# Performance work log

Measured on AMD Instinct MI355X. Metric: run time of the kernel, lower is better.

The kernel has to match this reference:

```python
import jax, jax.numpy as jnp
import numpy as np
import math

N_HEAD = 16
D_MODEL = 1024
D_HEAD = 64
GRID = 28


def _alibi_slopes(heads):
    def pow2(n):
        start = 2 ** (-(2 ** (-(math.log2(n) - 3))))
        return [start * (start ** i) for i in range(n)]
    if math.log2(heads).is_integer():
        return pow2(heads)
    c = 2 ** math.floor(math.log2(heads))
    return pow2(c) + pow2(2 * c)[0::2][: heads - c]


def _teeth_bias(heads):
    # bias[i,j] = |i%14 - j%14| + |i//14 - j//14| (loop in get_bias overwrites the -|j-i| init)
    idx = np.arange(GRID)
    row, col = idx // 14, idx % 14
    b = np.abs(col[:, None] - col[None, :]) + np.abs(row[:, None] - row[None, :])  # [28,28]
    slopes = np.asarray(_alibi_slopes(heads), dtype=np.float32)  # [h]
    return jnp.asarray(slopes[:, None, None] * b[None].astype(np.float32))  # [h,28,28]


def _layer_norm(x, gamma, beta, eps=1e-5):
    mu = jnp.mean(x, axis=-1, keepdims=True)
    var = jnp.var(x, axis=-1, keepdims=True)
    return (x - mu) * jax.lax.rsqrt(var + eps) * gamma + beta


def setup_inputs() -> dict:
    key = jax.random.key(0)
    ks = jax.random.split(key, 6)
    s = 0.02
    return {
        "hidden": jax.random.normal(ks[0], (2048, GRID, D_MODEL), dtype=jnp.float32),
        "wq": jax.random.normal(ks[1], (D_MODEL, N_HEAD * D_HEAD), dtype=jnp.float32) * s,
        "wk": jax.random.normal(ks[2], (D_MODEL, N_HEAD * D_HEAD), dtype=jnp.float32) * s,
        "wv": jax.random.normal(ks[3], (D_MODEL, N_HEAD * D_HEAD), dtype=jnp.float32) * s,
        "wo": jax.random.normal(ks[4], (N_HEAD * D_HEAD, D_MODEL), dtype=jnp.float32) * s,
        "gamma": jnp.ones((D_MODEL,), dtype=jnp.float32),
        "beta": jnp.zeros((D_MODEL,), dtype=jnp.float32),
    }


def reference(hidden, wq, wk, wv, wo, gamma, beta):
    b, s, _ = hidden.shape
    # pre_lnorm: hidden is reassigned to LN(hidden); combined == hidden (memory=None)
    h = _layer_norm(hidden, gamma, beta)
    q = (h @ wq).reshape(b, s, N_HEAD, D_HEAD).transpose(0, 2, 1, 3)  # [b,h,s,d]
    k = (h @ wk).reshape(b, s, N_HEAD, D_HEAD).transpose(0, 2, 1, 3)
    v = (h @ wv).reshape(b, s, N_HEAD, D_HEAD).transpose(0, 2, 1, 3)
    # NOTE: original forward never applies atten_scale -> unscaled dots (faithful)
    scores = jnp.einsum("bhid,bhjd->bhij", q, k)
    scores = scores + _teeth_bias(N_HEAD)[None, :, :s, :s]
    attn = jax.nn.softmax(scores, axis=-1)
    ctx = jnp.einsum("bhij,bhjd->bhid", attn, v)
    ctx = ctx.transpose(0, 2, 1, 3).reshape(b, s, N_HEAD * D_HEAD)
    out = ctx @ wo
    return h + out  # pre_lnorm residual uses the normalized hidden
```

## Files before the change

### kernel.cpp

```cpp
#include <hip/hip_runtime.h>
#include <hip/hip_bf16.h>

typedef unsigned short u16;
typedef __attribute__((ext_vector_type(8))) short bf16x8;
typedef __attribute__((ext_vector_type(4))) float f32x4;

#define DEVINL __device__ __forceinline__

DEVINL u16 f2b(float f) {
    __hip_bfloat16 h = __float2bfloat16(f);
    return __builtin_bit_cast(u16, h);
}
DEVINL float b2f(u16 u) {
    unsigned int x = ((unsigned int)u) << 16;
    return __builtin_bit_cast(float, x);
}
DEVINL int iabs(int x) { return x < 0 ? -x : x; }

#define GL2LDS(g, s)                                                                     \
    __builtin_amdgcn_global_load_lds(                                                    \
        (const __attribute__((address_space(1))) unsigned int*)(g),                      \
        (__attribute__((address_space(3))) unsigned int*)(s), 16, 0, 0)

__global__ __launch_bounds__(256) void wconv_kernel(const float* __restrict__ wq,
                                                    const float* __restrict__ wk,
                                                    const float* __restrict__ wv,
                                                    const float* __restrict__ wo,
                                                    u16* __restrict__ wqkvt,
                                                    u16* __restrict__ wot) {
    __shared__ float tile[32][33];
    int z = blockIdx.z;
    const float* src = (z == 0) ? wq : (z == 1) ? wk : (z == 2) ? wv : wo;
    int n0 = blockIdx.x * 32, k0 = blockIdx.y * 32;
    int r0 = threadIdx.x >> 5, c = threadIdx.x & 31;
#pragma unroll
    for (int i = 0; i < 4; i++) {
        int r = r0 + i * 8;
        tile[r][c] = src[(size_t)(k0 + r) * 1024 + n0 + c];
    }
    __syncthreads();
    u16* dst = (z < 3) ? (wqkvt + (size_t)z * 1024 * 1024) : wot;
#pragma unroll
    for (int i = 0; i < 4; i++) {
        int r = r0 + i * 8;
        dst[(size_t)(n0 + r) * 1024 + k0 + c] = f2b(tile[c][r]);
    }
}

__global__ __launch_bounds__(256) void ln_kernel(const float* __restrict__ x,
                                                 const float* __restrict__ gamma,
                                                 const float* __restrict__ beta,
                                                 u16* __restrict__ h) {
    int w = threadIdx.x >> 6, l = threadIdx.x & 63;
    size_t row = (size_t)blockIdx.x * 4 + w;
    const float4* xr = (const float4*)(x + row * 1024);
    float4 v[4];
    float s = 0.f, sq = 0.f;
#pragma unroll
    for (int i = 0; i < 4; i++) {
        v[i] = xr[l + i * 64];
        s += v[i].x + v[i].y + v[i].z + v[i].w;
        sq += v[i].x * v[i].x + v[i].y * v[i].y + v[i].z * v[i].z + v[i].w * v[i].w;
    }
#pragma unroll
    for (int off = 1; off < 64; off <<= 1) {
        s += __shfl_xor(s, off);
        sq += __shfl_xor(sq, off);
    }
    float mu = s * (1.f / 1024.f);
    float var = sq * (1.f / 1024.f) - mu * mu;
    float rstd = rsqrtf(var + 1e-5f);
    const float4* g4 = (const float4*)gamma;
    const float4* b4 = (const float4*)beta;
#pragma unroll
    for (int i = 0; i < 4; i++) {
        float4 g = g4[l + i * 64], b = b4[l + i * 64];
        float y0 = (v[i].x - mu) * rstd * g.x + b.x;
        float y1 = (v[i].y - mu) * rstd * g.y + b.y;
        float y2 = (v[i].z - mu) * rstd * g.z + b.z;
        float y3 = (v[i].w - mu) * rstd * g.w + b.w;
        unsigned int lo = (unsigned int)f2b(y0) | ((unsigned int)f2b(y1) << 16);
        unsigned int hi = (unsigned int)f2b(y2) | ((unsigned int)f2b(y3) << 16);
        uint2 pk;
        pk.x = lo;
        pk.y = hi;
        *(uint2*)(h + row * 1024 + (size_t)(l + i * 64) * 4) = pk;
    }
}

template <int OUT_BF16, int RESID>
__global__ __launch_bounds__(256, 2) void gemm_bt(const u16* __restrict__ A,
                                                  const u16* __restrict__ Bt,
                                                  void* __restrict__ Cv,
                                                  const u16* __restrict__ resid,
                                                  int lda, int ldc) {
    __shared__ u16 smem[16384];
    int t = threadIdx.x;

    int nwg = gridDim.x;
    int cpx = nwg >> 3;
    int wg = (blockIdx.x & 7) * cpx + (blockIdx.x >> 3);
    const int sgrp = 448 * 8;
    int sn = wg / sgrp;
    int rem = wg - sn * sgrp;
    int bm = rem >> 3;
    int bn = sn * 8 + (rem & 7);

    const char* Ab = (const char*)A;
    const char* Bb = (const char*)Bt;
    size_t aoffg[4], boffg[4];
#pragma unroll
    for (int i = 0; i < 4; i++) {
        int p = t * 16 + i * 4096;
        int row = p >> 7;
        int colb = (p & 127) ^ ((row & 7) << 4);
        aoffg[i] = (size_t)(bm * 128 + row) * (size_t)lda * 2 + colb;
        boffg[i] = (size_t)(bn * 128 + row) * 2048 + colb;
    }
    char* sA = (char*)smem;
    char* sB = sA + 16384;

    int l = t & 63, w = t >> 6;
    int wm = w >> 1, wn = w & 1, g = l >> 4, lr = l & 15;
    int swz = (lr & 7) << 4;

    f32x4 acc[4][4];
#pragma unroll
    for (int m = 0; m < 4; m++)
#pragma unroll
        for (int n = 0; n < 4; n++) acc[m][n] = {0.f, 0.f, 0.f, 0.f};

    for (int kt = 0; kt < 16; ++kt) {
        int kb = kt * 128;
#pragma unroll
        for (int i = 0; i < 4; i++) GL2LDS(Ab + aoffg[i] + kb, sA + i * 4096 + t * 16);
#pragma unroll
        for (int i = 0; i < 4; i++) GL2LDS(Bb + boffg[i] + kb, sB + i * 4096 + t * 16);
        __syncthreads();
#pragma unroll
        for (int ks = 0; ks < 2; ++ks) {
            bf16x8 af[4], bfv[4];
#pragma unroll
            for (int m = 0; m < 4; m++)
                af[m] = *(const bf16x8*)(sA + (wm * 64 + m * 16 + lr) * 128 +
                                         ((ks * 64 + g * 16) ^ swz));
#pragma unroll
            for (int n = 0; n < 4; n++)
                bfv[n] = *(const bf16x8*)(sB + (wn * 64 + n * 16 + lr) * 128 +
                                          ((ks * 64 + g * 16) ^ swz));
#pragma unroll
            for (int m = 0; m < 4; m++)
#pragma unroll
                for (int n = 0; n < 4; n++)
                    acc[m][n] =
                        __builtin_amdgcn_mfma_f32_16x16x32_bf16(af[m], bfv[n], acc[m][n], 0, 0, 0);
        }
        __syncthreads();
    }

    size_t row0 = (size_t)bm * 128 + wm * 64;
    int col0 = bn * 128 + wn * 64;
    if (OUT_BF16) {
        u16* C = (u16*)Cv;
#pragma unroll
        for (int m = 0; m < 4; m++)
#pragma unroll
            for (int n = 0; n < 4; n++)
#pragma unroll
                for (int r = 0; r < 4; r++) {
                    size_t rr = row0 + m * 16 + g * 4 + r;
                    int cc = col0 + n * 16 + lr;
                    C[rr * (size_t)ldc + cc] = f2b(acc[m][n][r]);
                }
    } else {
        float* C = (float*)Cv;
#pragma unroll
        for (int m = 0; m < 4; m++)
#pragma unroll
            for (int n = 0; n < 4; n++)
#pragma unroll
                for (int r = 0; r < 4; r++) {
                    size_t rr = row0 + m * 16 + g * 4 + r;
                    int cc = col0 + n * 16 + lr;
                    float o = acc[m][n][r];
                    if (RESID) o += b2f(resid[rr * 1024 + cc]);
                    C[rr * (size_t)ldc + cc] = o;
                }
    }
}

__global__ __launch_bounds__(256) void attn_kernel(u16* __restrict__ qkv) {
    __shared__ u16 sq[32][264];
    __shared__ u16 sk[32][264];
    __shared__ u16 svt[256][40];
    __shared__ u16 sp[4][32][40];

    int t = threadIdx.x;
    int b = blockIdx.x >> 2, hg = blockIdx.x & 3;
    u16* base = qkv + (size_t)b * 28 * 3072 + hg * 256;

    {
        int rhalf = t >> 7;
        int c2 = (t & 127) * 2;
        for (int it = 0; it < 14; ++it) {
            int row = it * 2 + rhalf;
            const u16* src = base + (size_t)row * 3072;
            unsigned int qv = *(const unsigned int*)(src + c2);
            *(unsigned int*)&sq[row][c2] = qv;
            unsigned int kv = *(const unsigned int*)(src + 1024 + c2);
            *(unsigned int*)&sk[row][c2] = kv;
            unsigned int vv = *(const unsigned int*)(src + 2048 + c2);
            svt[c2][row] = (u16)(vv & 0xffffu);
            svt[c2 + 1][row] = (u16)(vv >> 16);
        }
#pragma unroll
        for (int r = 28; r < 32; ++r) {
            sq[r][t] = 0;
            sk[r][t] = 0;
        }
#pragma unroll
        for (int j = 28; j < 32; ++j) svt[t][j] = 0;
    }
    __syncthreads();

    int w = t >> 6, l = t & 63, g = l >> 4, lr = l & 15;
    int head = hg * 4 + w;

    f32x4 acc[2][2];
#pragma unroll
    for (int a = 0; a < 2; a++)
#pragma unroll
        for (int c = 0; c < 2; c++) acc[a][c] = {0.f, 0.f, 0.f, 0.f};
#pragma unroll
    for (int c = 0; c < 2; c++) {
        int d0 = w * 64 + c * 32 + g * 8;
        bf16x8 a0 = *(const bf16x8*)&sq[lr][d0];
        bf16x8 a1 = *(const bf16x8*)&sq[16 + lr][d0];
        bf16x8 b0 = *(const bf16x8*)&sk[lr][d0];
        bf16x8 b1 = *(const bf16x8*)&sk[16 + lr][d0];
        acc[0][0] = __builtin_amdgcn_mfma_f32_16x16x32_bf16(a0, b0, acc[0][0], 0, 0, 0);
        acc[0][1] = __builtin_amdgcn_mfma_f32_16x16x32_bf16(a0, b1, acc[0][1], 0, 0, 0);
        acc[1][0] = __builtin_amdgcn_mfma_f32_16x16x32_bf16(a1, b0, acc[1][0], 0, 0, 0);
        acc[1][1] = __builtin_amdgcn_mfma_f32_16x16x32_bf16(a1, b1, acc[1][1], 0, 0, 0);
    }

    float slope = exp2f(-0.5f * (float)(head + 1));
    int j0 = lr, j1 = 16 + lr;
    int j0m = j0 % 14, j0d = j0 / 14;
    int j1m = j1 % 14, j1d = j1 / 14;
#pragma unroll
    for (int it = 0; it < 2; ++it) {
#pragma unroll
        for (int r = 0; r < 4; ++r) {
            int i = it * 16 + g * 4 + r;
            int im = i % 14, id = i / 14;
            float s0 = acc[it][0][r] + slope * (float)(iabs(im - j0m) + iabs(id - j0d));
            float s1 = (j1 < 28)
                           ? acc[it][1][r] + slope * (float)(iabs(im - j1m) + iabs(id - j1d))
                           : -1e30f;
            float mx = fmaxf(s0, s1);
#pragma unroll
            for (int off = 1; off < 16; off <<= 1) mx = fmaxf(mx, __shfl_xor(mx, off));
            float e0 = __expf(s0 - mx), e1 = __expf(s1 - mx);
            float sm = e0 + e1;
#pragma unroll
            for (int off = 1; off < 16; off <<= 1) sm += __shfl_xor(sm, off);
            float inv = 1.f / sm;
            sp[w][i][lr] = f2b(e0 * inv);
            sp[w][i][16 + lr] = f2b(e1 * inv);
        }
    }
    __syncthreads();

    bf16x8 pa0 = *(const bf16x8*)&sp[w][lr][g * 8];
    bf16x8 pa1 = *(const bf16x8*)&sp[w][16 + lr][g * 8];
    f32x4 o[2][4];
#pragma unroll
    for (int a = 0; a < 2; a++)
#pragma unroll
        for (int d = 0; d < 4; d++) o[a][d] = {0.f, 0.f, 0.f, 0.f};
#pragma unroll
    for (int dt = 0; dt < 4; ++dt) {
        bf16x8 bv = *(const bf16x8*)&svt[w * 64 + dt * 16 + lr][g * 8];
        o[0][dt] = __builtin_amdgcn_mfma_f32_16x16x32_bf16(pa0, bv, o[0][dt], 0, 0, 0);
        o[1][dt] = __builtin_amdgcn_mfma_f32_16x16x32_bf16(pa1, bv, o[1][dt], 0, 0, 0);
    }
#pragma unroll
    for (int it = 0; it < 2; ++it)
#pragma unroll
        for (int dt = 0; dt < 4; ++dt)
#pragma unroll
            for (int r = 0; r < 4; ++r) {
                int i = it * 16 + g * 4 + r;
                if (i < 28) {
                    size_t off = (size_t)(b * 28 + i) * 3072 + hg * 256 + w * 64 + dt * 16 + lr;
                    qkv[off] = f2b(o[it][dt][r]);
                }
            }
}

extern "C" void kernel_launch(void* const* d_in, const int* in_sizes, int n_in,
                              void* d_out, int out_size, void* d_ws, size_t ws_size,
                              hipStream_t stream) {
    (void)in_sizes; (void)n_in; (void)out_size; (void)ws_size;
    const float* hidden = (const float*)d_in[0];
    const float* wq = (const float*)d_in[1];
    const float* wk = (const float*)d_in[2];
    const float* wv = (const float*)d_in[3];
    const float* wo = (const float*)d_in[4];
    const float* gamma = (const float*)d_in[5];
    const float* beta = (const float*)d_in[6];
    float* out = (float*)d_out;

    char* ws = (char*)d_ws;
    u16* h = (u16*)ws;
    u16* qkv = (u16*)(ws + 117440512);
    u16* wqkvt = (u16*)(ws + 117440512 + 352321536);
    u16* wot = (u16*)(ws + 117440512 + 352321536 + 6291456);

    wconv_kernel<<<dim3(32, 32, 4), 256, 0, stream>>>(wq, wk, wv, wo, wqkvt, wot);
    ln_kernel<<<14336, 256, 0, stream>>>(hidden, gamma, beta, h);
    gemm_bt<1, 0><<<448 * 24, 256, 0, stream>>>(h, wqkvt, qkv, nullptr, 1024, 3072);
    attn_kernel<<<8192, 256, 0, stream>>>(qkv);
    gemm_bt<0, 1><<<448 * 8, 256, 0, stream>>>(qkv, wot, out, h, 3072, 1024);
}
```

Baseline: 698.4 us.

## Use 256x256 GEMM tiles with 8 waves and double-buffered LDS prefetch

The bf16 GEMM moves from 128x128 tiles with 4 waves to 256x256 tiles with 8 waves, which doubles operand reuse per loaded byte. LDS is now double-buffered (128 KB): loads for the next k-tile go directly to LDS and are interleaved between groups of MFMAs, so each iteration needs one barrier instead of two. s_setprio is raised around the MFMA groups to favour matrix issue. The cost is heavy LDS and register use, which allows only one workgroup per CU, plus fewer workgroups overall and a larger tail effect.

```diff
diff --git a/kernel.cpp b/kernel.cpp
--- a/kernel.cpp
+++ b/kernel.cpp
@@ -16,6 +16,9 @@
     return __builtin_bit_cast(float, x);
 }
 DEVINL int iabs(int x) { return x < 0 ? -x : x; }
+DEVINL f32x4 MFMA(bf16x8 a, bf16x8 b, f32x4 c) {
+    return __builtin_amdgcn_mfma_f32_16x16x32_bf16(a, b, c, 0, 0, 0);
+}
 
 #define GL2LDS(g, s)                                                                     \
     __builtin_amdgcn_global_load_lds(                                                    \
@@ -89,103 +92,174 @@
 }
 
 template <int OUT_BF16, int RESID>
-__global__ __launch_bounds__(256, 2) void gemm_bt(const u16* __restrict__ A,
-                                                  const u16* __restrict__ Bt,
-                                                  void* __restrict__ Cv,
-                                                  const u16* __restrict__ resid,
-                                                  int lda, int ldc) {
-    __shared__ u16 smem[16384];
+__global__ __launch_bounds__(512, 2) void gemm8(const u16* __restrict__ A,
+                                                const u16* __restrict__ Bt,
+                                                void* __restrict__ Cv,
+                                                const u16* __restrict__ resid,
+                                                int lda, int ldc) {
+    __shared__ u16 smem[65536];
     int t = threadIdx.x;
 
     int nwg = gridDim.x;
     int cpx = nwg >> 3;
-    int wg = (blockIdx.x & 7) * cpx + (blockIdx.x >> 3);
-    const int sgrp = 448 * 8;
-    int sn = wg / sgrp;
-    int rem = wg - sn * sgrp;
-    int bm = rem >> 3;
-    int bn = sn * 8 + (rem & 7);
-
-    const char* Ab = (const char*)A;
-    const char* Bb = (const char*)Bt;
-    size_t aoffg[4], boffg[4];
-#pragma unroll
-    for (int i = 0; i < 4; i++) {
-        int p = t * 16 + i * 4096;
-        int row = p >> 7;
-        int colb = (p & 127) ^ ((row & 7) << 4);
-        aoffg[i] = (size_t)(bm * 128 + row) * (size_t)lda * 2 + colb;
-        boffg[i] = (size_t)(bn * 128 + row) * 2048 + colb;
-    }
-    char* sA = (char*)smem;
-    char* sB = sA + 16384;
+    int wg = ((int)blockIdx.x & 7) * cpx + ((int)blockIdx.x >> 3);
+    int sn = wg / 896;
+    int rem = wg - sn * 896;
+    int bm = rem >> 2;
+    int bn = sn * 4 + (rem & 3);
+
+    int p16 = t * 16;
+    int srow = p16 >> 7;
+    int scolb = (p16 & 127) ^ ((srow & 7) << 4);
+    const char* aP = (const char*)A + (size_t)(bm * 256 + srow) * ((size_t)lda * 2) + scolb;
+    const char* bP = (const char*)Bt + (size_t)(bn * 256 + srow) * 2048 + scolb;
+    const size_t aStep = (size_t)lda * 2 * 64;
+    const size_t bStep = (size_t)2048 * 64;
+    char* sbase = (char*)smem;
 
     int l = t & 63, w = t >> 6;
-    int wm = w >> 1, wn = w & 1, g = l >> 4, lr = l & 15;
+    int wm = w >> 2, wn = w & 3, g = l >> 4, lr = l & 15;
     int swz = (lr & 7) << 4;
-
-    f32x4 acc[4][4];
-#pragma unroll
-    for (int m = 0; m < 4; m++)
+    int ldsoff = lr * 128 + ((g * 16) ^ swz);
+
+    f32x4 acc[8][4];
+#pragma unroll
+    for (int m = 0; m < 8; m++)
 #pragma unroll
         for (int n = 0; n < 4; n++) acc[m][n] = {0.f, 0.f, 0.f, 0.f};
 
-    for (int kt = 0; kt < 16; ++kt) {
-        int kb = kt * 128;
-#pragma unroll
-        for (int i = 0; i < 4; i++) GL2LDS(Ab + aoffg[i] + kb, sA + i * 4096 + t * 16);
-#pragma unroll
-        for (int i = 0; i < 4; i++) GL2LDS(Bb + boffg[i] + kb, sB + i * 4096 + t * 16);
+#pragma unroll
+    for (int i = 0; i < 4; i++) GL2LDS(aP + i * aStep, sbase + i * 8192 + p16);
+#pragma unroll
+    for (int i = 0; i < 4; i++) GL2LDS(bP + i * bStep, sbase + 32768 + i * 8192 + p16);
+    __syncthreads();
+
+#pragma unroll 1
+    for (int tk = 0; tk < 16; ++tk) {
+        const char* sA = sbase + (tk & 1) * 65536;
+        const char* sAw = sA + wm * 16384;
+        const char* sBw = sA + 32768 + wn * 8192;
+        char* sd = sbase + ((tk & 1) ^ 1) * 65536;
+        size_t kb = (size_t)(tk + 1) * 128;
+        bool st = tk < 15;
+
+        bf16x8 af[4][2], b0[2][2], b1[2][2];
+
+#pragma unroll
+        for (int m = 0; m < 4; m++)
+#pragma unroll
+            for (int ks = 0; ks < 2; ks++)
+                af[m][ks] = *(const bf16x8*)(sAw + m * 2048 + (ldsoff ^ (ks << 6)));
+#pragma unroll
+        for (int n = 0; n < 2; n++)
+#pragma unroll
+            for (int ks = 0; ks < 2; ks++)
+                b0[n][ks] = *(const bf16x8*)(sBw + n * 2048 + (ldsoff ^ (ks << 6)));
+        if (st) {
+            GL2LDS(aP + kb, sd + p16);
+            GL2LDS(aP + aStep + kb, sd + 8192 + p16);
+        }
+        __builtin_amdgcn_s_setprio(1);
+#pragma unroll
+        for (int m = 0; m < 4; m++)
+#pragma unroll
+            for (int n = 0; n < 2; n++)
+#pragma unroll
+                for (int ks = 0; ks < 2; ks++)
+                    acc[m][n] = MFMA(af[m][ks], b0[n][ks], acc[m][n]);
+        __builtin_amdgcn_s_setprio(0);
+
+#pragma unroll
+        for (int n = 0; n < 2; n++)
+#pragma unroll
+            for (int ks = 0; ks < 2; ks++)
+                b1[n][ks] = *(const bf16x8*)(sBw + 4096 + n * 2048 + (ldsoff ^ (ks << 6)));
+        if (st) {
+            GL2LDS(aP + 2 * aStep + kb, sd + 16384 + p16);
+            GL2LDS(aP + 3 * aStep + kb, sd + 24576 + p16);
+        }
+        __builtin_amdgcn_s_setprio(1);
+#pragma unroll
+        for (int m = 0; m < 4; m++)
+#pragma unroll
+            for (int n = 0; n < 2; n++)
+#pragma unroll
+                for (int ks = 0; ks < 2; ks++)
+                    acc[m][2 + n] = MFMA(af[m][ks], b1[n][ks], acc[m][2 + n]);
+        __builtin_amdgcn_s_setprio(0);
+
+#pragma unroll
+        for (int m = 0; m < 4; m++)
+#pragma unroll
+            for (int ks = 0; ks < 2; ks++)
+                af[m][ks] = *(const bf16x8*)(sAw + 8192 + m * 2048 + (ldsoff ^ (ks << 6)));
+        if (st) {
+            GL2LDS(bP + kb, sd + 32768 + p16);
+            GL2LDS(bP + bStep + kb, sd + 40960 + p16);
+        }
+        __builtin_amdgcn_s_setprio(1);
+#pragma unroll
+        for (int m = 0; m < 4; m++)
+#pragma unroll
+            for (int n = 0; n < 2; n++)
+#pragma unroll
+                for (int ks = 0; ks < 2; ks++)
+                    acc[4 + m][2 + n] = MFMA(af[m][ks], b1[n][ks], acc[4 + m][2 + n]);
+        __builtin_amdgcn_s_setprio(0);
+
+        if (st) {
+            GL2LDS(bP + 2 * bStep + kb, sd + 49152 + p16);
+            GL2LDS(bP + 3 * bStep + kb, sd + 57344 + p16);
+        }
+        __builtin_amdgcn_s_setprio(1);
+#pragma unroll
+        for (int m = 0; m < 4; m++)
+#pragma unroll
+            for (int n = 0; n < 2; n++)
+#pragma unroll
+                for (int ks = 0; ks < 2; ks++)
+                    acc[4 + m][n] = MFMA(af[m][ks], b0[n][ks], acc[4 + m][n]);
+        __builtin_amdgcn_s_setprio(0);
+
         __syncthreads();
-#pragma unroll
-        for (int ks = 0; ks < 2; ++ks) {
-            bf16x8 af[4], bfv[4];
-#pragma unroll
-            for (int m = 0; m < 4; m++)
-                af[m] = *(const bf16x8*)(sA + (wm * 64 + m * 16 + lr) * 128 +
-                                         ((ks * 64 + g * 16) ^ swz));
-#pragma unroll
-            for (int n = 0; n < 4; n++)
-                bfv[n] = *(const bf16x8*)(sB + (wn * 64 + n * 16 + lr) * 128 +
-                                          ((ks * 64 + g * 16) ^ swz));
-#pragma unroll
-            for (int m = 0; m < 4; m++)
-#pragma unroll
-                for (int n = 0; n < 4; n++)
-                    acc[m][n] =
-                        __builtin_amdgcn_mfma_f32_16x16x32_bf16(af[m], bfv[n], acc[m][n], 0, 0, 0);
-        }
-        __syncthreads();
-    }
-
-    size_t row0 = (size_t)bm * 128 + wm * 64;
-    int col0 = bn * 128 + wn * 64;
+    }
+
+    int row0 = bm * 256 + wm * 128;
+    int col0 = bn * 256 + wn * 64;
     if (OUT_BF16) {
         u16* C = (u16*)Cv;
 #pragma unroll
-        for (int m = 0; m < 4; m++)
-#pragma unroll
-            for (int n = 0; n < 4; n++)
-#pragma unroll
-                for (int r = 0; r < 4; r++) {
-                    size_t rr = row0 + m * 16 + g * 4 + r;
-                    int cc = col0 + n * 16 + lr;
-                    C[rr * (size_t)ldc + cc] = f2b(acc[m][n][r]);
-                }
+        for (int qm = 0; qm < 2; qm++)
+#pragma unroll
+            for (int m = 0; m < 4; m++)
+#pragma unroll
+                for (int qn = 0; qn < 2; qn++)
+#pragma unroll
+                    for (int n = 0; n < 2; n++)
+#pragma unroll
+                        for (int r = 0; r < 4; r++) {
+                            size_t rr = (size_t)(row0 + qm * 64 + m * 16 + g * 4 + r);
+                            int cc = col0 + qn * 32 + n * 16 + lr;
+                            C[rr * (size_t)ldc + cc] = f2b(acc[qm * 4 + m][qn * 2 + n][r]);
+                        }
     } else {
         float* C = (float*)Cv;
 #pragma unroll
-        for (int m = 0; m < 4; m++)
-#pragma unroll
-            for (int n = 0; n < 4; n++)
-#pragma unroll
-                for (int r = 0; r < 4; r++) {
-                    size_t rr = row0 + m * 16 + g * 4 + r;
-                    int cc = col0 + n * 16 + lr;
-                    float o = acc[m][n][r];
-                    if (RESID) o += b2f(resid[rr * 1024 + cc]);
-                    C[rr * (size_t)ldc + cc] = o;
-                }
+        for (int qm = 0; qm < 2; qm++)
+#pragma unroll
+            for (int m = 0; m < 4; m++)
+#pragma unroll
+                for (int qn = 0; qn < 2; qn++)
+#pragma unroll
+                    for (int n = 0; n < 2; n++)
+#pragma unroll
+                        for (int r = 0; r < 4; r++) {
+                            size_t rr = (size_t)(row0 + qm * 64 + m * 16 + g * 4 + r);
+                            int cc = col0 + qn * 32 + n * 16 + lr;
+                            float o = acc[qm * 4 + m][qn * 2 + n][r];
+                            if (RESID) o += b2f(resid[rr * 1024 + cc]);
+                            C[rr * (size_t)ldc + cc] = o;
+                        }
     }
 }
 
@@ -238,10 +312,10 @@
         bf16x8 a1 = *(const bf16x8*)&sq[16 + lr][d0];
         bf16x8 b0 = *(const bf16x8*)&sk[lr][d0];
         bf16x8 b1 = *(const bf16x8*)&sk[16 + lr][d0];
-        acc[0][0] = __builtin_amdgcn_mfma_f32_16x16x32_bf16(a0, b0, acc[0][0], 0, 0, 0);
-        acc[0][1] = __builtin_amdgcn_mfma_f32_16x16x32_bf16(a0, b1, acc[0][1], 0, 0, 0);
-        acc[1][0] = __builtin_amdgcn_mfma_f32_16x16x32_bf16(a1, b0, acc[1][0], 0, 0, 0);
-        acc[1][1] = __builtin_amdgcn_mfma_f32_16x16x32_bf16(a1, b1, acc[1][1], 0, 0, 0);
+        acc[0][0] = MFMA(a0, b0, acc[0][0]);
+        acc[0][1] = MFMA(a0, b1, acc[0][1]);
+        acc[1][0] = MFMA(a1, b0, acc[1][0]);
+        acc[1][1] = MFMA(a1, b1, acc[1][1]);
     }
 
     float slope = exp2f(-0.5f * (float)(head + 1));
@@ -282,8 +356,8 @@
 #pragma unroll
     for (int dt = 0; dt < 4; ++dt) {
         bf16x8 bv = *(const bf16x8*)&svt[w * 64 + dt * 16 + lr][g * 8];
-        o[0][dt] = __builtin_amdgcn_mfma_f32_16x16x32_bf16(pa0, bv, o[0][dt], 0, 0, 0);
-        o[1][dt] = __builtin_amdgcn_mfma_f32_16x16x32_bf16(pa1, bv, o[1][dt], 0, 0, 0);
+        o[0][dt] = MFMA(pa0, bv, o[0][dt]);
+        o[1][dt] = MFMA(pa1, bv, o[1][dt]);
     }
 #pragma unroll
     for (int it = 0; it < 2; ++it)
@@ -320,7 +394,7 @@
 
     wconv_kernel<<<dim3(32, 32, 4), 256, 0, stream>>>(wq, wk, wv, wo, wqkvt, wot);
     ln_kernel<<<14336, 256, 0, stream>>>(hidden, gamma, beta, h);
-    gemm_bt<1, 0><<<448 * 24, 256, 0, stream>>>(h, wqkvt, qkv, nullptr, 1024, 3072);
+    gemm8<1, 0><<<224 * 12, 512, 0, stream>>>(h, wqkvt, qkv, nullptr, 1024, 3072);
     attn_kernel<<<8192, 256, 0, stream>>>(qkv);
-    gemm_bt<0, 1><<<448 * 8, 256, 0, stream>>>(qkv, wot, out, h, 3072, 1024);
-}
+    gemm8<0, 1><<<224 * 4, 512, 0, stream>>>(qkv, wot, out, h, 3072, 1024);
+}
```

Result: no change. 708.7 us (+1.5%).

## Fuse QKV projection GEMM with per-head attention in one kernel

Applied to the files above, without the earlier changes.

Replaces the separate QKV GEMM and attention kernels with one fused kernel. Each workgroup computes a 112-row (4 batch) by 192-column (one head's Q, K, V) tile, stages the results in LDS, and runs the small 28x28 attention directly, writing only the context. The weight conversion interleaves Q/K/V rows per head so that tile is contiguous. This removes the round trip of the large QKV intermediate through global memory. The cost is a smaller, less efficient GEMM tile with no double buffering, plus higher LDS use that may limit occupancy.

```diff
diff --git a/kernel.cpp b/kernel.cpp
--- a/kernel.cpp
+++ b/kernel.cpp
@@ -16,6 +16,9 @@
     return __builtin_bit_cast(float, x);
 }
 DEVINL int iabs(int x) { return x < 0 ? -x : x; }
+DEVINL f32x4 MFMA(bf16x8 a, bf16x8 b, f32x4 c) {
+    return __builtin_amdgcn_mfma_f32_16x16x32_bf16(a, b, c, 0, 0, 0);
+}
 
 #define GL2LDS(g, s)                                                                     \
     __builtin_amdgcn_global_load_lds(                                                    \
@@ -39,11 +42,14 @@
         tile[r][c] = src[(size_t)(k0 + r) * 1024 + n0 + c];
     }
     __syncthreads();
-    u16* dst = (z < 3) ? (wqkvt + (size_t)z * 1024 * 1024) : wot;
+    u16* dst = (z < 3) ? wqkvt : wot;
 #pragma unroll
     for (int i = 0; i < 4; i++) {
         int r = r0 + i * 8;
-        dst[(size_t)(n0 + r) * 1024 + k0 + c] = f2b(tile[c][r]);
+        int nn = n0 + r;
+        size_t drow = (z < 3) ? ((size_t)(nn >> 6) * 192 + (size_t)z * 64 + (nn & 63))
+                              : (size_t)nn;
+        dst[drow * 1024 + k0 + c] = f2b(tile[c][r]);
     }
 }
 
@@ -88,6 +94,171 @@
     }
 }
 
+__global__ __launch_bounds__(256, 2) void fused_qkv_attn(const u16* __restrict__ h,
+                                                         const u16* __restrict__ wqkvt,
+                                                         u16* __restrict__ ctx) {
+    __shared__ __align__(16) char smem[62272];
+    char* sA = smem;
+    char* sB = smem + 16384;
+    int t = threadIdx.x;
+
+    int nwg = gridDim.x;
+    int cpx = nwg >> 3;
+    int wg = ((int)blockIdx.x & 7) * cpx + ((int)blockIdx.x >> 3);
+    int bm = wg >> 4;
+    int head = wg & 15;
+
+    int p16 = t * 16;
+    int srow = p16 >> 7;
+    int scolb = (p16 & 127) ^ ((srow & 7) << 4);
+    const char* aB = (const char*)h + ((size_t)bm * 112 + srow) * 2048 + scolb;
+    const char* bB = (const char*)wqkvt + ((size_t)head * 192 + srow) * 2048 + scolb;
+
+    int l = t & 63, w = t >> 6, g = l >> 4, lr = l & 15;
+    int swz = (lr & 7) << 4;
+
+    f32x4 acc[7][3];
+#pragma unroll
+    for (int m = 0; m < 7; m++)
+#pragma unroll
+        for (int n = 0; n < 3; n++) acc[m][n] = {0.f, 0.f, 0.f, 0.f};
+
+#pragma unroll 1
+    for (int kt = 0; kt < 16; ++kt) {
+        int kb = kt * 128;
+#pragma unroll
+        for (int i = 0; i < 4; i++) GL2LDS(aB + (size_t)i * 65536 + kb, sA + i * 4096 + p16);
+#pragma unroll
+        for (int i = 0; i < 6; i++) GL2LDS(bB + (size_t)i * 65536 + kb, sB + i * 4096 + p16);
+        __syncthreads();
+#pragma unroll
+        for (int ks = 0; ks < 2; ++ks) {
+            bf16x8 af[7], bfv[3];
+#pragma unroll
+            for (int m = 0; m < 7; m++)
+                af[m] = *(const bf16x8*)(sA + (m * 16 + lr) * 128 + ((ks * 64 + g * 16) ^ swz));
+#pragma unroll
+            for (int n = 0; n < 3; n++)
+                bfv[n] = *(const bf16x8*)(sB + (w * 48 + n * 16 + lr) * 128 +
+                                          ((ks * 64 + g * 16) ^ swz));
+#pragma unroll
+            for (int m = 0; m < 7; m++)
+#pragma unroll
+                for (int n = 0; n < 3; n++) acc[m][n] = MFMA(af[m], bfv[n], acc[m][n]);
+        }
+        __syncthreads();
+    }
+
+    u16(*qkb)[136] = (u16(*)[136])smem;
+    u16(*vt)[64][40] = (u16(*)[64][40])(smem + 31552);
+    u16(*sp)[32][40] = (u16(*)[32][40])(smem + 52032);
+
+    if (t < 136) {
+#pragma unroll
+        for (int r = 112; r < 116; ++r) qkb[r][t] = 0;
+    }
+    {
+        int s2 = t >> 6, d = t & 63;
+#pragma unroll
+        for (int j = 28; j < 32; ++j) vt[s2][d][j] = 0;
+    }
+#pragma unroll
+    for (int m = 0; m < 7; m++)
+#pragma unroll
+        for (int n = 0; n < 3; n++) {
+            int col = w * 48 + n * 16 + lr;
+#pragma unroll
+            for (int r = 0; r < 4; ++r) {
+                int row = m * 16 + g * 4 + r;
+                u16 val = f2b(acc[m][n][r]);
+                if (col < 128) {
+                    qkb[row][col] = val;
+                } else {
+                    int d = col - 128;
+                    int s2 = row / 28;
+                    int j = row - s2 * 28;
+                    vt[s2][d][j] = val;
+                }
+            }
+        }
+    __syncthreads();
+
+    int rbase = w * 28;
+    f32x4 sc[2][2];
+#pragma unroll
+    for (int a = 0; a < 2; a++)
+#pragma unroll
+        for (int c = 0; c < 2; c++) sc[a][c] = {0.f, 0.f, 0.f, 0.f};
+#pragma unroll
+    for (int c = 0; c < 2; c++) {
+        int off = c * 64 + g * 16;
+        const char* r0p = (const char*)&qkb[rbase + lr][0];
+        const char* r1p = (const char*)&qkb[rbase + 16 + lr][0];
+        bf16x8 a0 = *(const bf16x8*)(r0p + off);
+        bf16x8 a1 = *(const bf16x8*)(r1p + off);
+        bf16x8 b0 = *(const bf16x8*)(r0p + 128 + off);
+        bf16x8 b1 = *(const bf16x8*)(r1p + 128 + off);
+        sc[0][0] = MFMA(a0, b0, sc[0][0]);
+        sc[0][1] = MFMA(a0, b1, sc[0][1]);
+        sc[1][0] = MFMA(a1, b0, sc[1][0]);
+        sc[1][1] = MFMA(a1, b1, sc[1][1]);
+    }
+
+    float slope = exp2f(-0.5f * (float)(head + 1));
+    int j0 = lr, j1 = 16 + lr;
+    int j0m = j0 % 14, j0d = j0 / 14;
+    int j1m = j1 % 14, j1d = j1 / 14;
+#pragma unroll
+    for (int it = 0; it < 2; ++it) {
+#pragma unroll
+        for (int r = 0; r < 4; ++r) {
+            int i = it * 16 + g * 4 + r;
+            int im = i % 14, id = i / 14;
+            float s0 = sc[it][0][r] + slope * (float)(iabs(im - j0m) + iabs(id - j0d));
+            float s1 = (j1 < 28)
+                           ? sc[it][1][r] + slope * (float)(iabs(im - j1m) + iabs(id - j1d))
+                           : -1e30f;
+            float mx = fmaxf(s0, s1);
+#pragma unroll
+            for (int off = 1; off < 16; off <<= 1) mx = fmaxf(mx, __shfl_xor(mx, off));
+            float e0 = __expf(s0 - mx), e1 = __expf(s1 - mx);
+            float sm = e0 + e1;
+#pragma unroll
+            for (int off = 1; off < 16; off <<= 1) sm += __shfl_xor(sm, off);
+            float inv = 1.f / sm;
+            sp[w][i][lr] = f2b(e0 * inv);
+            sp[w][i][16 + lr] = f2b(e1 * inv);
+        }
+    }
+
+    bf16x8 pa0 = *(const bf16x8*)&sp[w][lr][g * 8];
+    bf16x8 pa1 = *(const bf16x8*)&sp[w][16 + lr][g * 8];
+    f32x4 o[2][4];
+#pragma unroll
+    for (int a = 0; a < 2; a++)
+#pragma unroll
+        for (int d = 0; d < 4; d++) o[a][d] = {0.f, 0.f, 0.f, 0.f};
+#pragma unroll
+    for (int dt = 0; dt < 4; ++dt) {
+        bf16x8 bv = *(const bf16x8*)&vt[w][dt * 16 + lr][g * 8];
+        o[0][dt] = MFMA(pa0, bv, o[0][dt]);
+        o[1][dt] = MFMA(pa1, bv, o[1][dt]);
+    }
+#pragma unroll
+    for (int it = 0; it < 2; ++it)
+#pragma unroll
+        for (int dt = 0; dt < 4; ++dt)
+#pragma unroll
+            for (int r = 0; r < 4; ++r) {
+                int i = it * 16 + g * 4 + r;
+                if (i < 28) {
+                    size_t off =
+                        ((size_t)(bm * 4 + w) * 28 + i) * 1024 + head * 64 + dt * 16 + lr;
+                    ctx[off] = f2b(o[it][dt][r]);
+                }
+            }
+}
+
 template <int OUT_BF16, int RESID>
 __global__ __launch_bounds__(256, 2) void gemm_bt(const u16* __restrict__ A,
                                                   const u16* __restrict__ Bt,
@@ -152,8 +323,7 @@
             for (int m = 0; m < 4; m++)
 #pragma unroll
                 for (int n = 0; n < 4; n++)
-                    acc[m][n] =
-                        __builtin_amdgcn_mfma_f32_16x16x32_bf16(af[m], bfv[n], acc[m][n], 0, 0, 0);
+                    acc[m][n] = MFMA(af[m], bfv[n], acc[m][n]);
         }
         __syncthreads();
     }
@@ -187,116 +357,6 @@
                     C[rr * (size_t)ldc + cc] = o;
                 }
     }
-}
-
-__global__ __launch_bounds__(256) void attn_kernel(u16* __restrict__ qkv) {
-    __shared__ u16 sq[32][264];
-    __shared__ u16 sk[32][264];
-    __shared__ u16 svt[256][40];
-    __shared__ u16 sp[4][32][40];
-
-    int t = threadIdx.x;
-    int b = blockIdx.x >> 2, hg = blockIdx.x & 3;
-    u16* base = qkv + (size_t)b * 28 * 3072 + hg * 256;
-
-    {
-        int rhalf = t >> 7;
-        int c2 = (t & 127) * 2;
-        for (int it = 0; it < 14; ++it) {
-            int row = it * 2 + rhalf;
-            const u16* src = base + (size_t)row * 3072;
-            unsigned int qv = *(const unsigned int*)(src + c2);
-            *(unsigned int*)&sq[row][c2] = qv;
-            unsigned int kv = *(const unsigned int*)(src + 1024 + c2);
-            *(unsigned int*)&sk[row][c2] = kv;
-            unsigned int vv = *(const unsigned int*)(src + 2048 + c2);
-            svt[c2][row] = (u16)(vv & 0xffffu);
-            svt[c2 + 1][row] = (u16)(vv >> 16);
-        }
-#pragma unroll
-        for (int r = 28; r < 32; ++r) {
-            sq[r][t] = 0;
-            sk[r][t] = 0;
-        }
-#pragma unroll
-        for (int j = 28; j < 32; ++j) svt[t][j] = 0;
-    }
-    __syncthreads();
-
-    int w = t >> 6, l = t & 63, g = l >> 4, lr = l & 15;
-    int head = hg * 4 + w;
-
-    f32x4 acc[2][2];
-#pragma unroll
-    for (int a = 0; a < 2; a++)
-#pragma unroll
-        for (int c = 0; c < 2; c++) acc[a][c] = {0.f, 0.f, 0.f, 0.f};
-#pragma unroll
-    for (int c = 0; c < 2; c++) {
-        int d0 = w * 64 + c * 32 + g * 8;
-        bf16x8 a0 = *(const bf16x8*)&sq[lr][d0];
-        bf16x8 a1 = *(const bf16x8*)&sq[16 + lr][d0];
-        bf16x8 b0 = *(const bf16x8*)&sk[lr][d0];
-        bf16x8 b1 = *(const bf16x8*)&sk[16 + lr][d0];
-        acc[0][0] = __builtin_amdgcn_mfma_f32_16x16x32_bf16(a0, b0, acc[0][0], 0, 0, 0);
-        acc[0][1] = __builtin_amdgcn_mfma_f32_16x16x32_bf16(a0, b1, acc[0][1], 0, 0, 0);
-        acc[1][0] = __builtin_amdgcn_mfma_f32_16x16x32_bf16(a1, b0, acc[1][0], 0, 0, 0);
-        acc[1][1] = __builtin_amdgcn_mfma_f32_16x16x32_bf16(a1, b1, acc[1][1], 0, 0, 0);
-    }
-
-    float slope = exp2f(-0.5f * (float)(head + 1));
-    int j0 = lr, j1 = 16 + lr;
-    int j0m = j0 % 14, j0d = j0 / 14;
-    int j1m = j1 % 14, j1d = j1 / 14;
-#pragma unroll
-    for (int it = 0; it < 2; ++it) {
-#pragma unroll
-        for (int r = 0; r < 4; ++r) {
-            int i = it * 16 + g * 4 + r;
-            int im = i % 14, id = i / 14;
-            float s0 = acc[it][0][r] + slope * (float)(iabs(im - j0m) + iabs(id - j0d));
-            float s1 = (j1 < 28)
-                           ? acc[it][1][r] + slope * (float)(iabs(im - j1m) + iabs(id - j1d))
-                           : -1e30f;
-            float mx = fmaxf(s0, s1);
-#pragma unroll
-            for (int off = 1; off < 16; off <<= 1) mx = fmaxf(mx, __shfl_xor(mx, off));
-            float e0 = __expf(s0 - mx), e1 = __expf(s1 - mx);
-            float sm = e0 + e1;
-#pragma unroll
-            for (int off = 1; off < 16; off <<= 1) sm += __shfl_xor(sm, off);
-            float inv = 1.f / sm;
-            sp[w][i][lr] = f2b(e0 * inv);
-            sp[w][i][16 + lr] = f2b(e1 * inv);
-        }
-    }
-    __syncthreads();
-
-    bf16x8 pa0 = *(const bf16x8*)&sp[w][lr][g * 8];
-    bf16x8 pa1 = *(const bf16x8*)&sp[w][16 + lr][g * 8];
-    f32x4 o[2][4];
-#pragma unroll
-    for (int a = 0; a < 2; a++)
-#pragma unroll
-        for (int d = 0; d < 4; d++) o[a][d] = {0.f, 0.f, 0.f, 0.f};
-#pragma unroll
-    for (int dt = 0; dt < 4; ++dt) {
-        bf16x8 bv = *(const bf16x8*)&svt[w * 64 + dt * 16 + lr][g * 8];
-        o[0][dt] = __builtin_amdgcn_mfma_f32_16x16x32_bf16(pa0, bv, o[0][dt], 0, 0, 0);
-        o[1][dt] = __builtin_amdgcn_mfma_f32_16x16x32_bf16(pa1, bv, o[1][dt], 0, 0, 0);
-    }
-#pragma unroll
-    for (int it = 0; it < 2; ++it)
-#pragma unroll
-        for (int dt = 0; dt < 4; ++dt)
-#pragma unroll
-            for (int r = 0; r < 4; ++r) {
-                int i = it * 16 + g * 4 + r;
-                if (i < 28) {
-                    size_t off = (size_t)(b * 28 + i) * 3072 + hg * 256 + w * 64 + dt * 16 + lr;
-                    qkv[off] = f2b(o[it][dt][r]);
-                }
-            }
 }
 
 extern "C" void kernel_launch(void* const* d_in, const int* in_sizes, int n_in,
@@ -314,13 +374,12 @@
 
     char* ws = (char*)d_ws;
     u16* h = (u16*)ws;
-    u16* qkv = (u16*)(ws + 117440512);
-    u16* wqkvt = (u16*)(ws + 117440512 + 352321536);
-    u16* wot = (u16*)(ws + 117440512 + 352321536 + 6291456);
+    u16* ctx = (u16*)(ws + 117440512);
+    u16* wqkvt = (u16*)(ws + 234881024);
+    u16* wot = (u16*)(ws + 234881024 + 6291456);
 
     wconv_kernel<<<dim3(32, 32, 4), 256, 0, stream>>>(wq, wk, wv, wo, wqkvt, wot);
     ln_kernel<<<14336, 256, 0, stream>>>(hidden, gamma, beta, h);
-    gemm_bt<1, 0><<<448 * 24, 256, 0, stream>>>(h, wqkvt, qkv, nullptr, 1024, 3072);
-    attn_kernel<<<8192, 256, 0, stream>>>(qkv);
-    gemm_bt<0, 1><<<448 * 8, 256, 0, stream>>>(qkv, wot, out, h, 3072, 1024);
-}
+    fused_qkv_attn<<<8192, 256, 0, stream>>>(h, wqkvt, ctx);
+    gemm_bt<0, 1><<<448 * 8, 256, 0, stream>>>(ctx, wot, out, h, 1024, 1024);
+}
```

Measured after the change: 754.4 us. +8.0%, slower.
